# Kernel tuning notes

Hardware: AMD Instinct MI355X
Metric: run time of the kernel (lower is better)

The kernel has to match this reference:

```python
import jax, jax.numpy as jnp
import numpy as np

B, N, F = 8, 2048, 128
H1, H2, D1 = 32, 64, 128


def setup_inputs() -> dict:
    key = jax.random.key(0)
    ks = jax.random.split(key, 10)
    x = jax.random.normal(ks[0], (B, N, F), dtype=jnp.float32)
    a = jax.random.uniform(ks[1], (B, N, N), dtype=jnp.float32)
    # GCN layer kernels (glorot-ish scale) and biases
    W1 = jax.random.normal(ks[2], (F, H1), dtype=jnp.float32) * (1.0 / np.sqrt(F))
    b1 = jnp.zeros((H1,), dtype=jnp.float32)
    W2 = jax.random.normal(ks[3], (H1, H2), dtype=jnp.float32) * (1.0 / np.sqrt(H1))
    b2 = jnp.zeros((H2,), dtype=jnp.float32)
    # Dense classifier after flatten: input dim = N * H2
    Wd = jax.random.normal(ks[4], (N * H2, D1), dtype=jnp.float32) * (1.0 / np.sqrt(N * H2))
    bd = jnp.zeros((D1,), dtype=jnp.float32)
    Wo = jax.random.normal(ks[5], (D1, 1), dtype=jnp.float32) * (1.0 / np.sqrt(D1))
    bo = jnp.zeros((1,), dtype=jnp.float32)
    return {"x": x, "a": a, "W1": W1, "b1": b1, "W2": W2, "b2": b2,
            "Wd": Wd, "bd": bd, "Wo": Wo, "bo": bo}


def reference(x, a, W1, b1, W2, b2, Wd, bd, Wo, bo):
    # GCNConv 1: relu(A @ (X @ W1) + b1)   [B,N,F] -> [B,N,H1]
    h = jax.nn.relu(jnp.einsum('bnm,bmh->bnh', a, x @ W1) + b1)
    # GCNConv 2: relu(A @ (H @ W2) + b2)   -> [B,N,H2]
    h = jax.nn.relu(jnp.einsum('bnm,bmh->bnh', a, h @ W2) + b2)
    # Flatten -> Dense(128, relu) -> (Dropout is identity at inference) -> Dense(1, sigmoid)
    h = h.reshape(h.shape[0], -1)          # [B, N*H2]
    h = jax.nn.relu(h @ Wd + bd)           # [B, D1]
    return jax.nn.sigmoid(h @ Wo + bo)     # [B, 1]
```

## Files before the change

kernel.cpp:

```cpp
#include <hip/hip_runtime.h>
#include <math.h>

#define B_  8
#define N_  2048
#define F_  128
#define H1_ 32
#define H2_ 64
#define D1_ 128
#define KS_ 4
#define KSEG_ (N_ / KS_)

typedef unsigned short u16;
typedef unsigned int   u32;
typedef __attribute__((ext_vector_type(8))) short short8;
typedef __attribute__((ext_vector_type(4))) float f32x4;

__device__ __forceinline__ u32 rne2(float e0, float e1) {
  u32 u0 = __float_as_uint(e0), u1 = __float_as_uint(e1);
  u0 = (u0 + 0x7FFFu + ((u0 >> 16) & 1u)) >> 16;
  u1 = (u1 + 0x7FFFu + ((u1 >> 16) & 1u)) & 0xFFFF0000u;
  return u0 | u1;
}
__device__ __forceinline__ uint4 rne8(const float4 a, const float4 b) {
  return make_uint4(rne2(a.x, a.y), rne2(a.z, a.w), rne2(b.x, b.y), rne2(b.z, b.w));
}

template<int H, int LDST>
__device__ __forceinline__ void pack_frags(const float* s, int b, int cgbase,
                                           u16* __restrict__ oh, int tid) {
  constexpr int CGRP = H / 16;
  constexpr int PASSES = H * 8 / 256;
#pragma unroll
  for (int p = 0; p < PASSES; ++p) {
    int q = tid + p * 256;
    int h = q >> 3, nn = (q & 7) * 8;
    u32 hw[4];
#pragma unroll
    for (int j = 0; j < 4; ++j)
      hw[j] = rne2(s[(nn + 2 * j) * LDST + h], s[(nn + 2 * j + 1) * LDST + h]);
    int ch = h >> 4, cl = h & 15;
    int cg = cgbase + (nn >> 5);
    int lanep = ((nn >> 3) & 3) * 16 + cl;
    size_t o = ((((size_t)b * CGRP + ch) * (N_ / 32) + cg) * 64 + lanep) * 8;
    *(uint4*)(oh + o) = make_uint4(hw[0], hw[1], hw[2], hw[3]);
  }
}

__global__ __launch_bounds__(256) void k_xw1cvt(const float* __restrict__ x,
                                                const float* __restrict__ W1,
                                                u16* __restrict__ oh) {
  __shared__ float xs[64][F_];
  __shared__ float w1s[F_ * H1_];
  __shared__ float s[64][H1_ + 1];
  const int b = blockIdx.y;
  const int n0 = blockIdx.x * 64;
  const int tid = threadIdx.x;
  const float* xp = x + ((size_t)b * N_ + n0) * F_;
#pragma unroll
  for (int i = 0; i < 8; ++i) {
    int q = tid + i * 256;
    int r = q >> 5, c4 = (q & 31) * 4;
    *(float4*)&xs[r][c4] = *(const float4*)(xp + (size_t)r * F_ + c4);
  }
#pragma unroll
  for (int i = 0; i < 4; ++i)
    ((float4*)w1s)[tid + i * 256] = ((const float4*)W1)[tid + i * 256];
  __syncthreads();
  const int r = tid >> 2, c0 = (tid & 3) * 8;
  float acc[8] = {};
#pragma unroll
  for (int k = 0; k < F_; ++k) {
    float xv = xs[r][k];
#pragma unroll
    for (int j = 0; j < 8; ++j)
      acc[j] = fmaf(xv, w1s[k * H1_ + c0 + j], acc[j]);
  }
#pragma unroll
  for (int j = 0; j < 8; ++j) s[r][c0 + j] = acc[j];
  __syncthreads();
  pack_frags<H1_, H1_ + 1>(&s[0][0], b, blockIdx.x * 2, oh, tid);
}

__global__ __launch_bounds__(256) void k_l1fuse(const float* __restrict__ P1,
                                                const float* __restrict__ b1,
                                                const float* __restrict__ W2,
                                                u16* __restrict__ oh) {
  __shared__ float h1s[64][H1_ + 1];
  __shared__ float w2s[H1_ * H2_];
  __shared__ float hw2s[64][H2_ + 1];
  const int b = blockIdx.y;
  const int n0 = blockIdx.x * 64;
  const int tid = threadIdx.x;
  constexpr size_t TOT = (size_t)B_ * N_ * H1_;
#pragma unroll
  for (int i = 0; i < 2; ++i) {
    int q = tid + i * 256;
    int r = q >> 3, h4 = (q & 7) * 4;
    size_t base = (((size_t)b * N_) + n0 + r) * H1_ + h4;
    float4 bv = *(const float4*)(b1 + h4);
    float a0 = bv.x, a1 = bv.y, a2 = bv.z, a3 = bv.w;
#pragma unroll
    for (int zz = 0; zz < KS_; ++zz) {
      float4 v = *(const float4*)(P1 + base + (size_t)zz * TOT);
      a0 += v.x; a1 += v.y; a2 += v.z; a3 += v.w;
    }
    h1s[r][h4 + 0] = fmaxf(a0, 0.f);
    h1s[r][h4 + 1] = fmaxf(a1, 0.f);
    h1s[r][h4 + 2] = fmaxf(a2, 0.f);
    h1s[r][h4 + 3] = fmaxf(a3, 0.f);
  }
#pragma unroll
  for (int i = 0; i < 2; ++i)
    ((float4*)w2s)[tid + i * 256] = ((const float4*)W2)[tid + i * 256];
  __syncthreads();
  const int r = tid >> 2, c0 = (tid & 3) * 16;
  float acc[16] = {};
#pragma unroll
  for (int k = 0; k < H1_; ++k) {
    float hv = h1s[r][k];
#pragma unroll
    for (int j = 0; j < 16; ++j)
      acc[j] = fmaf(hv, w2s[k * H2_ + c0 + j], acc[j]);
  }
#pragma unroll
  for (int j = 0; j < 16; ++j) hw2s[r][c0 + j] = acc[j];
  __syncthreads();
  pack_frags<H2_, H2_ + 1>(&hw2s[0][0], b, blockIdx.x * 2, oh, tid);
}

template<int H>
__global__ __launch_bounds__(256, 4) void k_agemm_mfma(const float* __restrict__ A,
                                                       const u16* __restrict__ Bph,
                                                       float* __restrict__ P) {
  constexpr int NT = H / 16;
  constexpr int BK = 64;
  constexpr int NTILE = KSEG_ / BK;
  constexpr int CHSTR = (N_ / 32) * 512;
  constexpr int BL = NT / 2;
  __shared__ u16 at[2][64][72];
  __shared__ u16 bt[2][2][NT][64][8];

  const int batch = blockIdx.y;
  const int z = blockIdx.z;
  const int m0 = blockIdx.x * 64;
  const int tid = threadIdx.x;
  const int lane = tid & 63;
  const int wave = tid >> 6;

  const float* Ab = A + (size_t)batch * N_ * N_ + (size_t)m0 * N_ + (size_t)z * KSEG_;
  const int srow = tid >> 2, sc0 = (tid & 3) * 16;

  const int cg0 = z * (KSEG_ / 32);
  const u16* Bb = Bph + (size_t)batch * NT * CHSTR;

  float4 sa[4];
  uint4  sb[BL];

#pragma unroll
  for (int i = 0; i < 4; ++i)
    sa[i] = *(const float4*)(Ab + (size_t)srow * N_ + sc0 + 4 * i);
#pragma unroll
  for (int i = 0; i < BL; ++i) {
    int q = tid + i * 256, seg = q >> 6, l2 = q & 63;
    int cc = seg / NT, ch = seg % NT;
    sb[i] = *(const uint4*)(Bb + (size_t)ch * CHSTR + (size_t)(cg0 + cc) * 512 + l2 * 8);
  }
  *(uint4*)&at[0][srow][sc0]     = rne8(sa[0], sa[1]);
  *(uint4*)&at[0][srow][sc0 + 8] = rne8(sa[2], sa[3]);
#pragma unroll
  for (int i = 0; i < BL; ++i) {
    int q = tid + i * 256, seg = q >> 6, l2 = q & 63;
    int cc = seg / NT, ch = seg % NT;
    *(uint4*)&bt[0][cc][ch][l2][0] = sb[i];
  }
  __syncthreads();

  f32x4 acc[NT];
#pragma unroll
  for (int c = 0; c < NT; ++c) acc[c] = (f32x4){0.f, 0.f, 0.f, 0.f};

  for (int t = 0; t < NTILE; ++t) {
    const int buf = t & 1;
    if (t + 1 < NTILE) {
      const int kk1 = (t + 1) * BK;
#pragma unroll
      for (int i = 0; i < 4; ++i)
        sa[i] = *(const float4*)(Ab + (size_t)srow * N_ + kk1 + sc0 + 4 * i);
#pragma unroll
      for (int i = 0; i < BL; ++i) {
        int q = tid + i * 256, seg = q >> 6, l2 = q & 63;
        int cc = seg / NT, ch = seg % NT;
        sb[i] = *(const uint4*)(Bb + (size_t)ch * CHSTR
                                + (size_t)(cg0 + 2 * (t + 1) + cc) * 512 + l2 * 8);
      }
      __builtin_amdgcn_sched_barrier(0);
    }
#pragma unroll
    for (int c = 0; c < 2; ++c) {
      short8 av = *(const short8*)&at[buf][wave * 16 + (lane & 15)][c * 32 + (lane >> 4) * 8];
#pragma unroll
      for (int ch = 0; ch < NT; ++ch) {
        short8 bv = *(const short8*)&bt[buf][c][ch][lane][0];
        acc[ch] = __builtin_amdgcn_mfma_f32_16x16x32_bf16(av, bv, acc[ch], 0, 0, 0);
      }
    }
    if (t + 1 < NTILE) {
      *(uint4*)&at[buf ^ 1][srow][sc0]     = rne8(sa[0], sa[1]);
      *(uint4*)&at[buf ^ 1][srow][sc0 + 8] = rne8(sa[2], sa[3]);
#pragma unroll
      for (int i = 0; i < BL; ++i) {
        int q = tid + i * 256, seg = q >> 6, l2 = q & 63;
        int cc = seg / NT, ch = seg % NT;
        *(uint4*)&bt[buf ^ 1][cc][ch][l2][0] = sb[i];
      }
    }
    __syncthreads();
  }
  const int orow = m0 + wave * 16 + ((lane >> 4) << 2);
  float* pp = P + ((size_t)(z * B_ + batch) * N_ + orow) * H + (lane & 15);
#pragma unroll
  for (int ch = 0; ch < NT; ++ch)
#pragma unroll
    for (int j = 0; j < 4; ++j)
      pp[(size_t)j * H + ch * 16] = acc[ch][j];
}

__global__ __launch_bounds__(512) void k_densefuse(const float* __restrict__ P2,
                                                   const float* __restrict__ b2,
                                                   const float* __restrict__ Wd,
                                                   float* __restrict__ part) {
  constexpr int KC = 512;
  __shared__ float hs[B_][KC];
  __shared__ float psum[B_][D1_];
  const int kc0 = blockIdx.x * KC;
  const int n0 = blockIdx.x * 8;
  const int tid = threadIdx.x;
  constexpr size_t TOT = (size_t)B_ * N_ * H2_;
#pragma unroll
  for (int i = 0; i < 2; ++i) {
    int q = tid + i * 512;
    int b = q >> 7, k4 = (q & 127) * 4;
    int nl = k4 >> 6, h = k4 & 63;
    size_t base = (((size_t)b * N_) + n0 + nl) * H2_ + h;
    float4 bv = *(const float4*)(b2 + h);
    float a0 = bv.x, a1 = bv.y, a2 = bv.z, a3 = bv.w;
#pragma unroll
    for (int zz = 0; zz < KS_; ++zz) {
      float4 v = *(const float4*)(P2 + base + (size_t)zz * TOT);
      a0 += v.x; a1 += v.y; a2 += v.z; a3 += v.w;
    }
    hs[b][k4 + 0] = fmaxf(a0, 0.f);
    hs[b][k4 + 1] = fmaxf(a1, 0.f);
    hs[b][k4 + 2] = fmaxf(a2, 0.f);
    hs[b][k4 + 3] = fmaxf(a3, 0.f);
  }
  __syncthreads();
  const int d0 = (tid & 31) * 4;
  const int b  = (tid >> 5) & 7;
  const int ks = tid >> 8;
  float a0 = 0.f, a1 = 0.f, a2 = 0.f, a3 = 0.f;
  const float* wp = Wd + ((size_t)kc0 + ks * 256) * D1_ + d0;
  const float* hp = &hs[b][ks * 256];
#pragma unroll 4
  for (int k = 0; k < 256; ++k) {
    float4 w = *(const float4*)(wp + (size_t)k * D1_);
    float h = hp[k];
    a0 = fmaf(h, w.x, a0); a1 = fmaf(h, w.y, a1);
    a2 = fmaf(h, w.z, a2); a3 = fmaf(h, w.w, a3);
  }
  if (ks == 1) {
    psum[b][d0] = a0; psum[b][d0 + 1] = a1; psum[b][d0 + 2] = a2; psum[b][d0 + 3] = a3;
  }
  __syncthreads();
  if (ks == 0) {
    float* pp = part + ((size_t)blockIdx.x * B_ + b) * D1_ + d0;
    *(float4*)pp = make_float4(a0 + psum[b][d0], a1 + psum[b][d0 + 1],
                               a2 + psum[b][d0 + 2], a3 + psum[b][d0 + 3]);
  }
}

__global__ __launch_bounds__(512) void k_dense_final(const float* __restrict__ part,
                                                     const float* __restrict__ bd,
                                                     const float* __restrict__ Wo,
                                                     const float* __restrict__ bo,
                                                     float* __restrict__ out) {
  __shared__ float ps[512];
  __shared__ float hdv[D1_];
  const int b = blockIdx.x;
  const int tid = threadIdx.x;
  const int d = tid & 127, seg = tid >> 7;
  float s = 0.f;
  for (int i = seg * 64; i < seg * 64 + 64; ++i)
    s += part[(size_t)i * (B_ * D1_) + b * D1_ + d];
  ps[tid] = s;
  __syncthreads();
  if (seg == 0)
    hdv[d] = fmaxf(ps[d] + ps[128 + d] + ps[256 + d] + ps[384 + d] + bd[d], 0.f);
  __syncthreads();
  if (tid < 64) {
    float v = hdv[tid] * Wo[tid] + hdv[64 + tid] * Wo[64 + tid];
#pragma unroll
    for (int off = 32; off; off >>= 1) v += __shfl_down(v, off, 64);
    if (tid == 0) out[b] = 1.f / (1.f + expf(-(v + bo[0])));
  }
}

extern "C" void kernel_launch(void* const* d_in, const int* in_sizes, int n_in,
                              void* d_out, int out_size, void* d_ws, size_t ws_size,
                              hipStream_t stream) {
  const float* x  = (const float*)d_in[0];
  const float* a  = (const float*)d_in[1];
  const float* W1 = (const float*)d_in[2];
  const float* b1 = (const float*)d_in[3];
  const float* W2 = (const float*)d_in[4];
  const float* b2 = (const float*)d_in[5];
  const float* Wd = (const float*)d_in[6];
  const float* bd = (const float*)d_in[7];
  const float* Wo = (const float*)d_in[8];
  const float* bo = (const float*)d_in[9];
  float* out = (float*)d_out;

  float* ws    = (float*)d_ws;
  float* P     = ws;
  u16*   Bt1h  = (u16*)(ws + 4194304);
  u16*   Bt2h  = (u16*)(ws + 4456448);
  float* dpart = ws + 4980736;

  k_xw1cvt<<<dim3(N_ / 64, B_), 256, 0, stream>>>(x, W1, Bt1h);
  k_agemm_mfma<H1_><<<dim3(N_ / 64, B_, KS_), 256, 0, stream>>>(a, Bt1h, P);
  k_l1fuse<<<dim3(N_ / 64, B_), 256, 0, stream>>>(P, b1, W2, Bt2h);
  k_agemm_mfma<H2_><<<dim3(N_ / 64, B_, KS_), 256, 0, stream>>>(a, Bt2h, P);
  k_densefuse<<<(N_ * H2_) / 512, 512, 0, stream>>>(P, b2, Wd, dpart);
  k_dense_final<<<B_, 512, 0, stream>>>(dpart, bd, Wo, bo, out);
}
```

Measured before the change: 108.2 us.

## Double A-GEMM block to 512 threads, splitting output columns across wave pairs

The A-matrix GEMM kernels now launch 512 threads per block instead of 256. Each of the 8 waves computes one 16-row group and half of the output column tiles. Each thread now stages half as much of the A tile and at most one B chunk per k-step. The goal is more waves in flight to hide the global loads of the large fp32 adjacency matrix. The cost is that every wave now reloads the A fragments and block-wide barriers are heavier.

After: 107.8 us. No clear change (-0.4%).

```diff
diff --git a/kernel.cpp b/kernel.cpp
--- a/kernel.cpp
+++ b/kernel.cpp
@@ -129,14 +129,15 @@
 }
 
 template<int H>
-__global__ __launch_bounds__(256, 4) void k_agemm_mfma(const float* __restrict__ A,
+__global__ __launch_bounds__(512, 8) void k_agemm_mfma(const float* __restrict__ A,
                                                        const u16* __restrict__ Bph,
                                                        float* __restrict__ P) {
   constexpr int NT = H / 16;
+  constexpr int NTW = NT / 2;
   constexpr int BK = 64;
   constexpr int NTILE = KSEG_ / BK;
   constexpr int CHSTR = (N_ / 32) * 512;
-  constexpr int BL = NT / 2;
+  constexpr int TOTB = 2 * NT * 64;
   __shared__ u16 at[2][64][72];
   __shared__ u16 bt[2][2][NT][64][8];
 
@@ -146,83 +147,67 @@
   const int tid = threadIdx.x;
   const int lane = tid & 63;
   const int wave = tid >> 6;
+  const int rg = wave & 3;
+  const int cb = (wave >> 2) * NTW;
 
   const float* Ab = A + (size_t)batch * N_ * N_ + (size_t)m0 * N_ + (size_t)z * KSEG_;
-  const int srow = tid >> 2, sc0 = (tid & 3) * 16;
+  const int srow = tid >> 3, sc0 = (tid & 7) * 8;
 
   const int cg0 = z * (KSEG_ / 32);
   const u16* Bb = Bph + (size_t)batch * NT * CHSTR;
-
-  float4 sa[4];
-  uint4  sb[BL];
-
-#pragma unroll
-  for (int i = 0; i < 4; ++i)
-    sa[i] = *(const float4*)(Ab + (size_t)srow * N_ + sc0 + 4 * i);
-#pragma unroll
-  for (int i = 0; i < BL; ++i) {
-    int q = tid + i * 256, seg = q >> 6, l2 = q & 63;
-    int cc = seg / NT, ch = seg % NT;
-    sb[i] = *(const uint4*)(Bb + (size_t)ch * CHSTR + (size_t)(cg0 + cc) * 512 + l2 * 8);
-  }
-  *(uint4*)&at[0][srow][sc0]     = rne8(sa[0], sa[1]);
-  *(uint4*)&at[0][srow][sc0 + 8] = rne8(sa[2], sa[3]);
-#pragma unroll
-  for (int i = 0; i < BL; ++i) {
-    int q = tid + i * 256, seg = q >> 6, l2 = q & 63;
-    int cc = seg / NT, ch = seg % NT;
-    *(uint4*)&bt[0][cc][ch][l2][0] = sb[i];
-  }
-  __syncthreads();
-
-  f32x4 acc[NT];
-#pragma unroll
-  for (int c = 0; c < NT; ++c) acc[c] = (f32x4){0.f, 0.f, 0.f, 0.f};
+  const int bseg = tid >> 6, bl2 = tid & 63;
+  const int bcc = bseg / NT, bch = bseg % NT;
+
+  float4 sa0, sa1;
+  uint4  sb;
+
+  sa0 = *(const float4*)(Ab + (size_t)srow * N_ + sc0);
+  sa1 = *(const float4*)(Ab + (size_t)srow * N_ + sc0 + 4);
+  if (tid < TOTB)
+    sb = *(const uint4*)(Bb + (size_t)bch * CHSTR + (size_t)(cg0 + bcc) * 512 + bl2 * 8);
+  *(uint4*)&at[0][srow][sc0] = rne8(sa0, sa1);
+  if (tid < TOTB)
+    *(uint4*)&bt[0][bcc][bch][bl2][0] = sb;
+  __syncthreads();
+
+  f32x4 acc[NTW];
+#pragma unroll
+  for (int c = 0; c < NTW; ++c) acc[c] = (f32x4){0.f, 0.f, 0.f, 0.f};
 
   for (int t = 0; t < NTILE; ++t) {
     const int buf = t & 1;
     if (t + 1 < NTILE) {
       const int kk1 = (t + 1) * BK;
-#pragma unroll
-      for (int i = 0; i < 4; ++i)
-        sa[i] = *(const float4*)(Ab + (size_t)srow * N_ + kk1 + sc0 + 4 * i);
-#pragma unroll
-      for (int i = 0; i < BL; ++i) {
-        int q = tid + i * 256, seg = q >> 6, l2 = q & 63;
-        int cc = seg / NT, ch = seg % NT;
-        sb[i] = *(const uint4*)(Bb + (size_t)ch * CHSTR
-                                + (size_t)(cg0 + 2 * (t + 1) + cc) * 512 + l2 * 8);
+      sa0 = *(const float4*)(Ab + (size_t)srow * N_ + kk1 + sc0);
+      sa1 = *(const float4*)(Ab + (size_t)srow * N_ + kk1 + sc0 + 4);
+      if (tid < TOTB)
+        sb = *(const uint4*)(Bb + (size_t)bch * CHSTR
+                             + (size_t)(cg0 + 2 * (t + 1) + bcc) * 512 + bl2 * 8);
+      __builtin_amdgcn_sched_barrier(0);
+    }
+#pragma unroll
+    for (int c = 0; c < 2; ++c) {
+      short8 av = *(const short8*)&at[buf][rg * 16 + (lane & 15)][c * 32 + (lane >> 4) * 8];
+#pragma unroll
+      for (int j = 0; j < NTW; ++j) {
+        short8 bv = *(const short8*)&bt[buf][c][cb + j][lane][0];
+        acc[j] = __builtin_amdgcn_mfma_f32_16x16x32_bf16(av, bv, acc[j], 0, 0, 0);
       }
-      __builtin_amdgcn_sched_barrier(0);
-    }
-#pragma unroll
-    for (int c = 0; c < 2; ++c) {
-      short8 av = *(const short8*)&at[buf][wave * 16 + (lane & 15)][c * 32 + (lane >> 4) * 8];
-#pragma unroll
-      for (int ch = 0; ch < NT; ++ch) {
-        short8 bv = *(const short8*)&bt[buf][c][ch][lane][0];
-        acc[ch] = __builtin_amdgcn_mfma_f32_16x16x32_bf16(av, bv, acc[ch], 0, 0, 0);
-      }
     }
     if (t + 1 < NTILE) {
-      *(uint4*)&at[buf ^ 1][srow][sc0]     = rne8(sa[0], sa[1]);
-      *(uint4*)&at[buf ^ 1][srow][sc0 + 8] = rne8(sa[2], sa[3]);
-#pragma unroll
-      for (int i = 0; i < BL; ++i) {
-        int q = tid + i * 256, seg = q >> 6, l2 = q & 63;
-        int cc = seg / NT, ch = seg % NT;
-        *(uint4*)&bt[buf ^ 1][cc][ch][l2][0] = sb[i];
-      }
+      *(uint4*)&at[buf ^ 1][srow][sc0] = rne8(sa0, sa1);
+      if (tid < TOTB)
+        *(uint4*)&bt[buf ^ 1][bcc][bch][bl2][0] = sb;
     }
     __syncthreads();
   }
-  const int orow = m0 + wave * 16 + ((lane >> 4) << 2);
-  float* pp = P + ((size_t)(z * B_ + batch) * N_ + orow) * H + (lane & 15);
-#pragma unroll
-  for (int ch = 0; ch < NT; ++ch)
-#pragma unroll
-    for (int j = 0; j < 4; ++j)
-      pp[(size_t)j * H + ch * 16] = acc[ch][j];
+  const int orow = m0 + rg * 16 + ((lane >> 4) << 2);
+  float* pp = P + ((size_t)(z * B_ + batch) * N_ + orow) * H + cb * 16 + (lane & 15);
+#pragma unroll
+  for (int j = 0; j < NTW; ++j)
+#pragma unroll
+    for (int jj = 0; jj < 4; ++jj)
+      pp[(size_t)jj * H + j * 16] = acc[j][jj];
 }
 
 __global__ __launch_bounds__(512) void k_densefuse(const float* __restrict__ P2,
@@ -327,9 +312,9 @@
   float* dpart = ws + 4980736;
 
   k_xw1cvt<<<dim3(N_ / 64, B_), 256, 0, stream>>>(x, W1, Bt1h);
-  k_agemm_mfma<H1_><<<dim3(N_ / 64, B_, KS_), 256, 0, stream>>>(a, Bt1h, P);
+  k_agemm_mfma<H1_><<<dim3(N_ / 64, B_, KS_), 512, 0, stream>>>(a, Bt1h, P);
   k_l1fuse<<<dim3(N_ / 64, B_), 256, 0, stream>>>(P, b1, W2, Bt2h);
-  k_agemm_mfma<H2_><<<dim3(N_ / 64, B_, KS_), 256, 0, stream>>>(a, Bt2h, P);
+  k_agemm_mfma<H2_><<<dim3(N_ / 64, B_, KS_), 512, 0, stream>>>(a, Bt2h, P);
   k_densefuse<<<(N_ * H2_) / 512, 512, 0, stream>>>(P, b2, Wd, dpart);
   k_dense_final<<<B_, 512, 0, stream>>>(dpart, bd, Wo, bo, out);
 }
```
